# Kernel tuning notes

Measured on AMD Instinct MI355X. Metric: run time of the kernel, lower is better.

## Reference

```python
import jax, jax.numpy as jnp
import numpy as np

B, S, D, H = 4, 2048, 1024, 16
DK = D // H

def setup_inputs() -> dict:
    key = jax.random.key(0)
    ks = jax.random.split(key, 8)
    Q = jax.random.normal(ks[0], (B, S, D), dtype=jnp.float32)
    K = jax.random.normal(ks[1], (B, S, D), dtype=jnp.float32)
    V = jax.random.normal(ks[2], (B, S, D), dtype=jnp.float32)
    # causal mask: 0 means masked (as in masked_fill(mask == 0, -inf))
    mask = jnp.broadcast_to(jnp.tril(jnp.ones((S, S), dtype=jnp.int32))[None, None], (B, 1, S, S))
    scale = 1.0 / np.sqrt(D)
    W_Q = jax.random.normal(ks[3], (D, D), dtype=jnp.float32) * scale
    W_K = jax.random.normal(ks[4], (D, D), dtype=jnp.float32) * scale
    W_V = jax.random.normal(ks[5], (D, D), dtype=jnp.float32) * scale
    W_O = jax.random.normal(ks[6], (D, D), dtype=jnp.float32) * scale
    return {"Q": Q, "K": K, "V": V, "mask": mask,
            "W_Q": W_Q, "W_K": W_K, "W_V": W_V, "W_O": W_O}

def _split_heads(x):
    # [B, S, D] -> [B, H, S, DK]
    b, s, _ = x.shape
    return x.reshape(b, s, H, DK).transpose(0, 2, 1, 3)

def reference(Q, K, V, mask, W_Q, W_K, W_V, W_O):
    # nn.Linear(d,d,bias=False): y = x @ W.T ; here W_* stored as [D, D]
    q = _split_heads(Q @ W_Q.T)
    k = _split_heads(K @ W_K.T)
    v = _split_heads(V @ W_V.T)
    scores = jnp.einsum('bhqd,bhkd->bhqk', q, k) / jnp.sqrt(jnp.float32(DK))
    scores = jnp.where(mask == 0, -jnp.inf, scores)
    weights = jax.nn.softmax(scores, axis=-1)
    weights = jnp.nan_to_num(weights, nan=0.0)  # fully-masked rows -> 0
    # dropout is identity at eval / p=0
    attn = jnp.einsum('bhqk,bhkd->bhqd', weights, v)
    attn = attn.transpose(0, 2, 1, 3).reshape(Q.shape[0], Q.shape[1], D)
    return attn @ W_O.T
```

## Files before the change

### kernel.cpp

```cpp
#include <hip/hip_runtime.h>
#include <stdint.h>

#define B_  4
#define S_  2048
#define D_  1024
#define H_  16
#define DK_ 64

typedef __attribute__((ext_vector_type(8)))  short   short8;
typedef __attribute__((ext_vector_type(8)))  unsigned short ushort8;
typedef __attribute__((ext_vector_type(4)))  float   f32x4;
typedef __attribute__((ext_vector_type(16))) float   f32x16;

#define GPTR(p) ((const __attribute__((address_space(1))) void*)(p))
#define SPTR(p) ((__attribute__((address_space(3))) void*)(p))

__device__ inline unsigned short f2bf(float f) {
  uint32_t u = __float_as_uint(f);
  uint32_t r = (u + 0x7fffu + ((u >> 16) & 1u)) >> 16;
  return (unsigned short)r;
}
__device__ inline float bf2f(unsigned short h) {
  return __uint_as_float(((uint32_t)h) << 16);
}
__device__ inline uint32_t pkbf(float a, float b) {
  uint32_t r;
  asm("v_cvt_pk_bf16_f32 %0, %1, %2" : "=v"(r) : "v"(a), "v"(b));
  return r;
}
__device__ inline void pl32(uint32_t& a, uint32_t& b) {
  asm volatile("v_permlane32_swap_b32 %0, %1" : "+v"(a), "+v"(b));
}
__device__ inline short8 mk8(uint32_t a, uint32_t b, uint32_t c, uint32_t d) {
  union { uint32_t u[4]; short8 s; } x;
  x.u[0] = a; x.u[1] = b; x.u[2] = c; x.u[3] = d;
  return x.s;
}

__global__ __launch_bounds__(256) void conv_one(const float* __restrict__ src,
                                                unsigned short* __restrict__ dst,
                                                size_t n) {
  size_t i = ((size_t)blockIdx.x * blockDim.x + threadIdx.x) * 4;
  if (i < n) {
    float4 v = *reinterpret_cast<const float4*>(src + i);
    ushort4 o;
    o.x = f2bf(v.x); o.y = f2bf(v.y); o.z = f2bf(v.z); o.w = f2bf(v.w);
    *reinterpret_cast<ushort4*>(dst + i) = o;
  }
}

__global__ __launch_bounds__(256) void conv_x3(const float* __restrict__ q,
                                               const float* __restrict__ k,
                                               const float* __restrict__ v,
                                               unsigned short* __restrict__ dst) {
  const size_t NX = (size_t)B_ * S_ * D_;
  const float* src = (blockIdx.z == 0) ? q : (blockIdx.z == 1) ? k : v;
  unsigned short* d = dst + (size_t)blockIdx.z * NX;
  size_t i = ((size_t)blockIdx.x * blockDim.x + threadIdx.x) * 4;
  float4 vv = *reinterpret_cast<const float4*>(src + i);
  ushort4 o;
  o.x = f2bf(vv.x); o.y = f2bf(vv.y); o.z = f2bf(vv.z); o.w = f2bf(vv.w);
  *reinterpret_cast<ushort4*>(d + i) = o;
}

__global__ __launch_bounds__(256) void conv_w4(const float* __restrict__ w0,
                                               const float* __restrict__ w1,
                                               const float* __restrict__ w2,
                                               const float* __restrict__ w3,
                                               unsigned short* __restrict__ dst) {
  const size_t NW = (size_t)D_ * D_;
  const float* src = (blockIdx.z == 0) ? w0 : (blockIdx.z == 1) ? w1
                   : (blockIdx.z == 2) ? w2 : w3;
  unsigned short* d = dst + (size_t)blockIdx.z * NW;
  size_t i = ((size_t)blockIdx.x * blockDim.x + threadIdx.x) * 4;
  if (i < NW) {
    float4 v = *reinterpret_cast<const float4*>(src + i);
    ushort4 o;
    o.x = f2bf(v.x); o.y = f2bf(v.y); o.z = f2bf(v.z); o.w = f2bf(v.w);
    *reinterpret_cast<ushort4*>(d + i) = o;
  }
}

#define BM 128
#define BN 128
#define BK 32

__global__ __launch_bounds__(256) void gemm_qkv(const unsigned short* __restrict__ X0,
                                                const unsigned short* __restrict__ X1,
                                                const unsigned short* __restrict__ X2,
                                                const unsigned short* __restrict__ W,
                                                unsigned short* __restrict__ P,
                                                int zbase) {
  const size_t NW = (size_t)D_ * D_;
  const size_t NX = (size_t)B_ * S_ * D_;
  const int z = zbase + blockIdx.z;

  const unsigned short* A;
  const unsigned short* Bm;
  unsigned short* C;
  int N, m0, n0;
  if (z == 2) {
    A = W + 2 * NW; Bm = X2; C = P + 2 * NX;
    N = B_ * S_;
    m0 = (blockIdx.x & 7) * BM;
    n0 = (blockIdx.x >> 3) * BN;
  } else {
    A = z ? X1 : X0; Bm = W + (size_t)z * NW; C = P + (size_t)z * NX;
    N = D_;
    m0 = (blockIdx.x >> 3) * BM;
    n0 = (blockIdx.x & 7) * BN;
  }
  const int K = D_;

  __shared__ unsigned short sA[2][BM * BK];
  __shared__ unsigned short sB[2][BN * BK];

  const int tid  = threadIdx.x;
  const int lane = tid & 63;
  const int wid  = tid >> 6;
  const int wr   = wid >> 1, wc = wid & 1;
  const int g = lane >> 4, c = lane & 15;

  f32x4 acc[4][4];
#pragma unroll
  for (int m = 0; m < 4; ++m)
#pragma unroll
    for (int n = 0; n < 4; ++n) acc[m][n] = (f32x4){0.f, 0.f, 0.f, 0.f};

  auto stage = [&](int kt_, int bs) {
    const int k0 = kt_ * BK;
#pragma unroll
    for (int i = 0; i < 2; ++i) {
      const int ob  = i * 4096 + wid * 1024 + lane * 16;
      const int row = ob >> 6;
      const int cb  = ob & 63;
      const unsigned short* ga = A  + (size_t)(m0 + row) * K + k0 + (cb >> 1);
      const unsigned short* gb = Bm + (size_t)(n0 + row) * K + k0 + (cb >> 1);
      __builtin_amdgcn_global_load_lds(GPTR(ga), SPTR(&sA[bs][(i * 4096 + wid * 1024) >> 1]), 16, 0, 0);
      __builtin_amdgcn_global_load_lds(GPTR(gb), SPTR(&sB[bs][(i * 4096 + wid * 1024) >> 1]), 16, 0, 0);
    }
  };

  const int nkt = K / BK;
  stage(0, 0);
  __syncthreads();
  int cur = 0;
  for (int kt = 0; kt < nkt; ++kt) {
    if (kt + 1 < nkt) stage(kt + 1, cur ^ 1);

    short8 af[4], bf[4];
#pragma unroll
    for (int m = 0; m < 4; ++m)
      af[m] = *reinterpret_cast<const short8*>(&sA[cur][(wr * 64 + m * 16 + c) * BK + 8 * g]);
#pragma unroll
    for (int n = 0; n < 4; ++n)
      bf[n] = *reinterpret_cast<const short8*>(&sB[cur][(wc * 64 + n * 16 + c) * BK + 8 * g]);
#pragma unroll
    for (int m = 0; m < 4; ++m)
#pragma unroll
      for (int n = 0; n < 4; ++n)
        acc[m][n] = __builtin_amdgcn_mfma_f32_16x16x32_bf16(af[m], bf[n], acc[m][n], 0, 0, 0);
    __syncthreads();
    cur ^= 1;
  }

#pragma unroll
  for (int m = 0; m < 4; ++m)
#pragma unroll
    for (int n = 0; n < 4; ++n)
#pragma unroll
      for (int r = 0; r < 4; ++r) {
        const int row = m0 + wr * 64 + m * 16 + 4 * g + r;
        const int col = n0 + wc * 64 + n * 16 + c;
        C[(size_t)row * N + col] = f2bf(acc[m][n][r]);
      }
}

__global__ __launch_bounds__(256) void gemm_out(const unsigned short* __restrict__ A,
                                                const unsigned short* __restrict__ Bm,
                                                float* __restrict__ C,
                                                int M, int N, int K) {
  __shared__ unsigned short sA[2][BM * BK];
  __shared__ unsigned short sB[2][BN * BK];

  const int tid  = threadIdx.x;
  const int lane = tid & 63;
  const int wid  = tid >> 6;
  const int wr   = wid >> 1, wc = wid & 1;
  const int g = lane >> 4, c = lane & 15;

  const int m0 = blockIdx.y * BM;
  const int n0 = blockIdx.x * BN;

  f32x4 acc[4][4];
#pragma unroll
  for (int m = 0; m < 4; ++m)
#pragma unroll
    for (int n = 0; n < 4; ++n) acc[m][n] = (f32x4){0.f, 0.f, 0.f, 0.f};

  auto stage = [&](int kt_, int bs) {
    const int k0 = kt_ * BK;
#pragma unroll
    for (int i = 0; i < 2; ++i) {
      const int ob  = i * 4096 + wid * 1024 + lane * 16;
      const int row = ob >> 6;
      const int cb  = ob & 63;
      const unsigned short* ga = A  + (size_t)(m0 + row) * K + k0 + (cb >> 1);
      const unsigned short* gb = Bm + (size_t)(n0 + row) * K + k0 + (cb >> 1);
      __builtin_amdgcn_global_load_lds(GPTR(ga), SPTR(&sA[bs][(i * 4096 + wid * 1024) >> 1]), 16, 0, 0);
      __builtin_amdgcn_global_load_lds(GPTR(gb), SPTR(&sB[bs][(i * 4096 + wid * 1024) >> 1]), 16, 0, 0);
    }
  };

  const int nkt = K / BK;
  stage(0, 0);
  __syncthreads();
  int cur = 0;
  for (int kt = 0; kt < nkt; ++kt) {
    if (kt + 1 < nkt) stage(kt + 1, cur ^ 1);

    short8 af[4], bf[4];
#pragma unroll
    for (int m = 0; m < 4; ++m)
      af[m] = *reinterpret_cast<const short8*>(&sA[cur][(wr * 64 + m * 16 + c) * BK + 8 * g]);
#pragma unroll
    for (int n = 0; n < 4; ++n)
      bf[n] = *reinterpret_cast<const short8*>(&sB[cur][(wc * 64 + n * 16 + c) * BK + 8 * g]);
#pragma unroll
    for (int m = 0; m < 4; ++m)
#pragma unroll
      for (int n = 0; n < 4; ++n)
        acc[m][n] = __builtin_amdgcn_mfma_f32_16x16x32_bf16(af[m], bf[n], acc[m][n], 0, 0, 0);
    __syncthreads();
    cur ^= 1;
  }

#pragma unroll
  for (int m = 0; m < 4; ++m)
#pragma unroll
    for (int n = 0; n < 4; ++n)
#pragma unroll
      for (int r = 0; r < 4; ++r) {
        const int row = m0 + wr * 64 + m * 16 + 4 * g + r;
        const int col = n0 + wc * 64 + n * 16 + c;
        C[(size_t)row * N + col] = acc[m][n][r];
      }
}

__global__ __launch_bounds__(256, 4) void attn_fwd(const unsigned short* __restrict__ qp,
                                                   const unsigned short* __restrict__ kp,
                                                   const unsigned short* __restrict__ vtp,
                                                   unsigned short* __restrict__ attn) {
  const int bh = blockIdx.x;
  const int bx = blockIdx.y;
  const int b = bh >> 4, h = bh & 15;

  __shared__ unsigned short smem[4 * 64 * 64];

  const int tid  = threadIdx.x;
  const int lane = tid & 63;
  const int wid  = tid >> 6;
  const int hi   = lane >> 5;
  const int lo5  = lane & 31;

  const size_t headoff  = (size_t)b * S_ * D_ + (size_t)h * DK_;
  const size_t vheadoff = (size_t)(h * DK_) * (size_t)(B_ * S_) + (size_t)b * S_;

  const int xk = (lo5 & 7) << 4;

  auto stage = [&](int kt_, int bs) {
#pragma unroll
    for (int i = 0; i < 2; ++i) {
      const int base_ob = i * 4096 + wid * 1024;
      const int ob  = base_ob + lane * 16;
      const int row = ob >> 7;
      const int scb = (ob & 127) ^ ((row & 7) << 4);
      const unsigned short* gk = &kp[headoff + (size_t)(kt_ * 64 + row) * D_ + (scb >> 1)];
      const unsigned short* gv = &vtp[vheadoff + (size_t)row * (B_ * S_) + kt_ * 64 + (scb >> 1)];
      __builtin_amdgcn_global_load_lds(GPTR(gk), SPTR(&smem[bs * 4096 + (base_ob >> 1)]), 16, 0, 0);
      __builtin_amdgcn_global_load_lds(GPTR(gv), SPTR(&smem[8192 + bs * 4096 + (base_ob >> 1)]), 16, 0, 0);
    }
  };

#pragma unroll 1
  for (int pass = 0; pass < 2; ++pass) {
    const int qtile = pass ? bx : (15 - bx);
    const int qw = qtile * 128 + wid * 32;
    const int qg = qw + lo5;

    __syncthreads();

    short8 aq[4];
#pragma unroll
    for (int t = 0; t < 4; ++t) {
      ushort8 raw = *reinterpret_cast<const ushort8*>(
          &qp[headoff + (size_t)qg * D_ + t * 16 + hi * 8]);
      short8 sv;
#pragma unroll
      for (int j = 0; j < 8; ++j) sv[j] = (short)f2bf(bf2f(raw[j]) * 0.125f);
      aq[t] = sv;
    }

    float mrun = -3.0e38f, lrun = 0.f;
    f32x16 oa0, oa1;
#pragma unroll
    for (int r = 0; r < 16; ++r) { oa0[r] = 0.f; oa1[r] = 0.f; }

    const int nkv = 2 * (qtile + 1);
    stage(0, 0);

    for (int kt = 0; kt < nkv; ++kt) {
      const int cur = kt & 1;
      if (kt < nkv - 1) {
        stage(kt + 1, cur ^ 1);
        asm volatile("s_waitcnt vmcnt(4)" ::: "memory");
      } else {
        asm volatile("s_waitcnt vmcnt(0)" ::: "memory");
      }
      __builtin_amdgcn_sched_barrier(0);
      __builtin_amdgcn_s_barrier();
      __builtin_amdgcn_sched_barrier(0);

      const int kv0 = kt * 64;
      if (kv0 <= qw + 31) {
        const unsigned short* Kb = &smem[cur * 4096];
        const unsigned short* Vb = &smem[8192 + cur * 4096];

        f32x16 st0, st1;
#pragma unroll
        for (int r = 0; r < 16; ++r) { st0[r] = 0.f; st1[r] = 0.f; }
        __builtin_amdgcn_s_setprio(1);
#pragma unroll
        for (int t = 0; t < 4; ++t) {
          const int off = ((32 * t + 16 * hi) ^ xk) >> 1;
          short8 k0 = *reinterpret_cast<const short8*>(&Kb[lo5 * 64 + off]);
          short8 k1 = *reinterpret_cast<const short8*>(&Kb[(32 + lo5) * 64 + off]);
          st0 = __builtin_amdgcn_mfma_f32_32x32x16_bf16(k0, aq[t], st0, 0, 0, 0);
          st1 = __builtin_amdgcn_mfma_f32_32x32x16_bf16(k1, aq[t], st1, 0, 0, 0);
        }
        __builtin_amdgcn_s_setprio(0);

        if (kv0 + 63 > qw) {
#pragma unroll
          for (int r = 0; r < 16; ++r) {
            const int kvl = kv0 + (r & 3) + 8 * (r >> 2) + 4 * hi;
            if (kvl > qg)      st0[r] = -3.0e38f;
            if (kvl + 32 > qg) st1[r] = -3.0e38f;
          }
        }

        float tm = fmaxf(st0[0], st1[0]);
#pragma unroll
        for (int r = 1; r < 16; ++r) tm = fmaxf(tm, fmaxf(st0[r], st1[r]));
        tm = fmaxf(tm, __shfl_xor(tm, 32));
        const bool grow = !__all(tm <= mrun + 8.0f);
        float alpha = 1.0f;
        if (grow) {
          const float newm = fmaxf(mrun, tm);
          alpha = __expf(mrun - newm);
          mrun = newm;
        }

        float ls = 0.f;
#pragma unroll
        for (int r = 0; r < 16; ++r) { st0[r] = __expf(st0[r] - mrun); ls += st0[r]; }
        uint32_t a0 = pkbf(st0[0],  st0[1]),  a1 = pkbf(st0[2],  st0[3]);
        uint32_t b0 = pkbf(st0[4],  st0[5]),  b1 = pkbf(st0[6],  st0[7]);
        uint32_t c0 = pkbf(st0[8],  st0[9]),  c1 = pkbf(st0[10], st0[11]);
        uint32_t d0 = pkbf(st0[12], st0[13]), d1 = pkbf(st0[14], st0[15]);
        pl32(a0, b0); pl32(a1, b1);
        pl32(c0, d0); pl32(c1, d1);
        short8 pf0 = mk8(a0, a1, b0, b1);
        short8 pf1 = mk8(c0, c1, d0, d1);

#pragma unroll
        for (int r = 0; r < 16; ++r) { st1[r] = __expf(st1[r] - mrun); ls += st1[r]; }
        uint32_t e0 = pkbf(st1[0],  st1[1]),  e1 = pkbf(st1[2],  st1[3]);
        uint32_t f0 = pkbf(st1[4],  st1[5]),  f1 = pkbf(st1[6],  st1[7]);
        uint32_t g0 = pkbf(st1[8],  st1[9]),  g1 = pkbf(st1[10], st1[11]);
        uint32_t h0 = pkbf(st1[12], st1[13]), h1 = pkbf(st1[14], st1[15]);
        pl32(e0, f0); pl32(e1, f1);
        pl32(g0, h0); pl32(g1, h1);
        short8 pf2 = mk8(e0, e1, f0, f1);
        short8 pf3 = mk8(g0, g1, h0, h1);

        ls += __shfl_xor(ls, 32);
        if (grow) {
          lrun = lrun * alpha + ls;
#pragma unroll
          for (int r = 0; r < 16; ++r) { oa0[r] *= alpha; oa1[r] *= alpha; }
        } else {
          lrun += ls;
        }

        __builtin_amdgcn_s_setprio(1);
#pragma unroll
        for (int c4 = 0; c4 < 4; ++c4) {
          const int off = ((32 * c4 + 16 * hi) ^ xk) >> 1;
          short8 v0 = *reinterpret_cast<const short8*>(&Vb[lo5 * 64 + off]);
          short8 v1 = *reinterpret_cast<const short8*>(&Vb[(32 + lo5) * 64 + off]);
          const short8 pf = (c4 == 0) ? pf0 : (c4 == 1) ? pf1 : (c4 == 2) ? pf2 : pf3;
          oa0 = __builtin_amdgcn_mfma_f32_32x32x16_bf16(v0, pf, oa0, 0, 0, 0);
          oa1 = __builtin_amdgcn_mfma_f32_32x32x16_bf16(v1, pf, oa1, 0, 0, 0);
        }
        __builtin_amdgcn_s_setprio(0);
      }

      asm volatile("s_waitcnt lgkmcnt(0)" ::: "memory");
      __builtin_amdgcn_sched_barrier(0);
      __builtin_amdgcn_s_barrier();
      __builtin_amdgcn_sched_barrier(0);
    }

    {
      unsigned short* sO = &smem[wid * (32 * 72)];
      const float inv = 1.0f / lrun;
#pragma unroll
      for (int r = 0; r < 16; ++r) {
        const int dl = (r & 3) + 8 * (r >> 2) + 4 * hi;
        sO[lo5 * 72 + dl]      = f2bf(oa0[r] * inv);
        sO[lo5 * 72 + 32 + dl] = f2bf(oa1[r] * inv);
      }
      asm volatile("s_waitcnt lgkmcnt(0)" ::: "memory");
      const int row = lane >> 1, h2 = lane & 1;
      const unsigned short* src = &smem[wid * (32 * 72) + row * 72 + h2 * 32];
      unsigned short* dst = &attn[headoff + (size_t)(qtile * 128 + wid * 32 + row) * D_ + h2 * 32];
#pragma unroll
      for (int j = 0; j < 4; ++j)
        *reinterpret_cast<short8*>(dst + 8 * j) = *reinterpret_cast<const short8*>(src + 8 * j);
    }
  }
}

extern "C" void kernel_launch(void* const* d_in, const int* in_sizes, int n_in,
                              void* d_out, int out_size, void* d_ws, size_t ws_size,
                              hipStream_t stream) {
  const float* Q  = (const float*)d_in[0];
  const float* K  = (const float*)d_in[1];
  const float* V  = (const float*)d_in[2];
  const float* Wq = (const float*)d_in[4];
  const float* Wk = (const float*)d_in[5];
  const float* Wv = (const float*)d_in[6];
  const float* Wo = (const float*)d_in[7];
  float* out = (float*)d_out;

  const size_t NX = (size_t)B_ * S_ * D_;
  const size_t NW = (size_t)D_ * D_;

  const bool fused = ws_size >= 2 * (6 * NX + 4 * NW);

  unsigned short* ws = (unsigned short*)d_ws;
  unsigned short* Xq = ws;
  unsigned short* Xk = fused ? Xq + NX : Xq;
  unsigned short* Xv = fused ? Xk + NX : Xq;
  unsigned short* Wb = Xv + NX;
  unsigned short* Pj = Wb + 4 * NW;
  unsigned short* At = Xq;

  const int M = B_ * S_;
  dim3 blk(256);
  dim3 gridConvX((unsigned)(NX / 4 / 256), 1, 3);
  dim3 gridConvW((unsigned)(NW / 4 / 256), 1, 4);
  dim3 gridQKV(512, 1, 3);
  dim3 gridOut(D_ / BN, M / BM);
  dim3 gridAttn(B_ * H_, 8);

  conv_w4<<<gridConvW, blk, 0, stream>>>(Wq, Wk, Wv, Wo, Wb);

  if (fused) {
    conv_x3<<<gridConvX, blk, 0, stream>>>(Q, K, V, Xq);
    gemm_qkv<<<gridQKV, blk, 0, stream>>>(Xq, Xk, Xv, Wb, Pj, 0);
  } else {
    dim3 g1((unsigned)(NX / 4 / 256));
    dim3 gz(512, 1, 1);
    conv_one<<<g1, blk, 0, stream>>>(Q, Xq, NX);
    gemm_qkv<<<gz, blk, 0, stream>>>(Xq, Xq, Xq, Wb, Pj, 0);
    conv_one<<<g1, blk, 0, stream>>>(K, Xq, NX);
    gemm_qkv<<<gz, blk, 0, stream>>>(Xq, Xq, Xq, Wb, Pj, 1);
    conv_one<<<g1, blk, 0, stream>>>(V, Xq, NX);
    gemm_qkv<<<gz, blk, 0, stream>>>(Xq, Xq, Xq, Wb, Pj, 2);
  }

  attn_fwd<<<gridAttn, blk, 0, stream>>>(Pj, Pj + NX, Pj + 2 * NX, At);
  gemm_out<<<gridOut, blk, 0, stream>>>(At, Wb + 3 * NW, out, M, D_, D_);
}
```

Baseline: 208.9 us.

## Triple-buffer GEMM loads with explicit vmcnt waits, LDS swizzle, and block remap

Both bf16 GEMM kernels (QKV projection and output projection) move from a double-buffered to a triple-buffered global-to-LDS pipeline, prefetching two K-tiles ahead. Manual s_waitcnt vmcnt counts and raw s_barrier calls replace __syncthreads. An XOR swizzle on the LDS column chunk is meant to cut bank conflicts on the short8 fragment reads. MFMA sections run at raised wave priority, and the block index mapping is changed so consecutive blocks walk the M dimension, which alters L2 reuse of the weight tiles. The extra buffer raises LDS use per block, and the hand-counted vmcnt values must match the number of outstanding loads exactly.

```diff
diff --git a/kernel.cpp b/kernel.cpp
--- a/kernel.cpp
+++ b/kernel.cpp
@@ -102,18 +102,18 @@
   if (z == 2) {
     A = W + 2 * NW; Bm = X2; C = P + 2 * NX;
     N = B_ * S_;
-    m0 = (blockIdx.x & 7) * BM;
-    n0 = (blockIdx.x >> 3) * BN;
+    m0 = (blockIdx.x >> 6) * BM;
+    n0 = (blockIdx.x & 63) * BN;
   } else {
     A = z ? X1 : X0; Bm = W + (size_t)z * NW; C = P + (size_t)z * NX;
     N = D_;
-    m0 = (blockIdx.x >> 3) * BM;
-    n0 = (blockIdx.x & 7) * BN;
+    m0 = (blockIdx.x & 63) * BM;
+    n0 = (blockIdx.x >> 6) * BN;
   }
   const int K = D_;
 
-  __shared__ unsigned short sA[2][BM * BK];
-  __shared__ unsigned short sB[2][BN * BK];
+  __shared__ unsigned short sA[3][BM * BK];
+  __shared__ unsigned short sB[3][BN * BK];
 
   const int tid  = threadIdx.x;
   const int lane = tid & 63;
@@ -131,37 +131,59 @@
     const int k0 = kt_ * BK;
 #pragma unroll
     for (int i = 0; i < 2; ++i) {
-      const int ob  = i * 4096 + wid * 1024 + lane * 16;
+      const int base_ob = i * 4096 + wid * 1024;
+      const int ob  = base_ob + lane * 16;
       const int row = ob >> 6;
-      const int cb  = ob & 63;
-      const unsigned short* ga = A  + (size_t)(m0 + row) * K + k0 + (cb >> 1);
-      const unsigned short* gb = Bm + (size_t)(n0 + row) * K + k0 + (cb >> 1);
-      __builtin_amdgcn_global_load_lds(GPTR(ga), SPTR(&sA[bs][(i * 4096 + wid * 1024) >> 1]), 16, 0, 0);
-      __builtin_amdgcn_global_load_lds(GPTR(gb), SPTR(&sB[bs][(i * 4096 + wid * 1024) >> 1]), 16, 0, 0);
+      const int scb = (ob & 63) ^ (((ob >> 7) & 3) << 4);
+      const unsigned short* ga = A  + (size_t)(m0 + row) * K + k0 + (scb >> 1);
+      const unsigned short* gb = Bm + (size_t)(n0 + row) * K + k0 + (scb >> 1);
+      __builtin_amdgcn_global_load_lds(GPTR(ga), SPTR(&sA[bs][base_ob >> 1]), 16, 0, 0);
+      __builtin_amdgcn_global_load_lds(GPTR(gb), SPTR(&sB[bs][base_ob >> 1]), 16, 0, 0);
     }
   };
 
   const int nkt = K / BK;
   stage(0, 0);
-  __syncthreads();
-  int cur = 0;
+  stage(1, 1);
   for (int kt = 0; kt < nkt; ++kt) {
-    if (kt + 1 < nkt) stage(kt + 1, cur ^ 1);
+    const int cur = kt % 3;
+    if (kt + 2 < nkt) {
+      stage(kt + 2, (kt + 2) % 3);
+      asm volatile("s_waitcnt vmcnt(8)" ::: "memory");
+    } else if (kt + 1 < nkt) {
+      asm volatile("s_waitcnt vmcnt(4)" ::: "memory");
+    } else {
+      asm volatile("s_waitcnt vmcnt(0)" ::: "memory");
+    }
+    __builtin_amdgcn_sched_barrier(0);
+    __builtin_amdgcn_s_barrier();
+    __builtin_amdgcn_sched_barrier(0);
 
     short8 af[4], bf[4];
 #pragma unroll
-    for (int m = 0; m < 4; ++m)
-      af[m] = *reinterpret_cast<const short8*>(&sA[cur][(wr * 64 + m * 16 + c) * BK + 8 * g]);
-#pragma unroll
-    for (int n = 0; n < 4; ++n)
-      bf[n] = *reinterpret_cast<const short8*>(&sB[cur][(wc * 64 + n * 16 + c) * BK + 8 * g]);
+    for (int m = 0; m < 4; ++m) {
+      const int ra = wr * 64 + m * 16 + c;
+      af[m] = *reinterpret_cast<const short8*>(
+          &sA[cur][ra * BK + ((g ^ ((ra >> 1) & 3)) << 3)]);
+    }
+#pragma unroll
+    for (int n = 0; n < 4; ++n) {
+      const int rb = wc * 64 + n * 16 + c;
+      bf[n] = *reinterpret_cast<const short8*>(
+          &sB[cur][rb * BK + ((g ^ ((rb >> 1) & 3)) << 3)]);
+    }
+    __builtin_amdgcn_s_setprio(1);
 #pragma unroll
     for (int m = 0; m < 4; ++m)
 #pragma unroll
       for (int n = 0; n < 4; ++n)
         acc[m][n] = __builtin_amdgcn_mfma_f32_16x16x32_bf16(af[m], bf[n], acc[m][n], 0, 0, 0);
-    __syncthreads();
-    cur ^= 1;
+    __builtin_amdgcn_s_setprio(0);
+
+    asm volatile("s_waitcnt lgkmcnt(0)" ::: "memory");
+    __builtin_amdgcn_sched_barrier(0);
+    __builtin_amdgcn_s_barrier();
+    __builtin_amdgcn_sched_barrier(0);
   }
 
 #pragma unroll
@@ -180,8 +202,8 @@
                                                 const unsigned short* __restrict__ Bm,
                                                 float* __restrict__ C,
                                                 int M, int N, int K) {
-  __shared__ unsigned short sA[2][BM * BK];
-  __shared__ unsigned short sB[2][BN * BK];
+  __shared__ unsigned short sA[3][BM * BK];
+  __shared__ unsigned short sB[3][BN * BK];
 
   const int tid  = threadIdx.x;
   const int lane = tid & 63;
@@ -189,8 +211,8 @@
   const int wr   = wid >> 1, wc = wid & 1;
   const int g = lane >> 4, c = lane & 15;
 
-  const int m0 = blockIdx.y * BM;
-  const int n0 = blockIdx.x * BN;
+  const int m0 = blockIdx.x * BM;
+  const int n0 = blockIdx.y * BN;
 
   f32x4 acc[4][4];
 #pragma unroll
@@ -202,37 +224,59 @@
     const int k0 = kt_ * BK;
 #pragma unroll
     for (int i = 0; i < 2; ++i) {
-      const int ob  = i * 4096 + wid * 1024 + lane * 16;
+      const int base_ob = i * 4096 + wid * 1024;
+      const int ob  = base_ob + lane * 16;
       const int row = ob >> 6;
-      const int cb  = ob & 63;
-      const unsigned short* ga = A  + (size_t)(m0 + row) * K + k0 + (cb >> 1);
-      const unsigned short* gb = Bm + (size_t)(n0 + row) * K + k0 + (cb >> 1);
-      __builtin_amdgcn_global_load_lds(GPTR(ga), SPTR(&sA[bs][(i * 4096 + wid * 1024) >> 1]), 16, 0, 0);
-      __builtin_amdgcn_global_load_lds(GPTR(gb), SPTR(&sB[bs][(i * 4096 + wid * 1024) >> 1]), 16, 0, 0);
+      const int scb = (ob & 63) ^ (((ob >> 7) & 3) << 4);
+      const unsigned short* ga = A  + (size_t)(m0 + row) * K + k0 + (scb >> 1);
+      const unsigned short* gb = Bm + (size_t)(n0 + row) * K + k0 + (scb >> 1);
+      __builtin_amdgcn_global_load_lds(GPTR(ga), SPTR(&sA[bs][base_ob >> 1]), 16, 0, 0);
+      __builtin_amdgcn_global_load_lds(GPTR(gb), SPTR(&sB[bs][base_ob >> 1]), 16, 0, 0);
     }
   };
 
   const int nkt = K / BK;
   stage(0, 0);
-  __syncthreads();
-  int cur = 0;
+  stage(1, 1);
   for (int kt = 0; kt < nkt; ++kt) {
-    if (kt + 1 < nkt) stage(kt + 1, cur ^ 1);
+    const int cur = kt % 3;
+    if (kt + 2 < nkt) {
+      stage(kt + 2, (kt + 2) % 3);
+      asm volatile("s_waitcnt vmcnt(8)" ::: "memory");
+    } else if (kt + 1 < nkt) {
+      asm volatile("s_waitcnt vmcnt(4)" ::: "memory");
+    } else {
+      asm volatile("s_waitcnt vmcnt(0)" ::: "memory");
+    }
+    __builtin_amdgcn_sched_barrier(0);
+    __builtin_amdgcn_s_barrier();
+    __builtin_amdgcn_sched_barrier(0);
 
     short8 af[4], bf[4];
 #pragma unroll
-    for (int m = 0; m < 4; ++m)
-      af[m] = *reinterpret_cast<const short8*>(&sA[cur][(wr * 64 + m * 16 + c) * BK + 8 * g]);
-#pragma unroll
-    for (int n = 0; n < 4; ++n)
-      bf[n] = *reinterpret_cast<const short8*>(&sB[cur][(wc * 64 + n * 16 + c) * BK + 8 * g]);
+    for (int m = 0; m < 4; ++m) {
+      const int ra = wr * 64 + m * 16 + c;
+      af[m] = *reinterpret_cast<const short8*>(
+          &sA[cur][ra * BK + ((g ^ ((ra >> 1) & 3)) << 3)]);
+    }
+#pragma unroll
+    for (int n = 0; n < 4; ++n) {
+      const int rb = wc * 64 + n * 16 + c;
+      bf[n] = *reinterpret_cast<const short8*>(
+          &sB[cur][rb * BK + ((g ^ ((rb >> 1) & 3)) << 3)]);
+    }
+    __builtin_amdgcn_s_setprio(1);
 #pragma unroll
     for (int m = 0; m < 4; ++m)
 #pragma unroll
       for (int n = 0; n < 4; ++n)
         acc[m][n] = __builtin_amdgcn_mfma_f32_16x16x32_bf16(af[m], bf[n], acc[m][n], 0, 0, 0);
-    __syncthreads();
-    cur ^= 1;
+    __builtin_amdgcn_s_setprio(0);
+
+    asm volatile("s_waitcnt lgkmcnt(0)" ::: "memory");
+    __builtin_amdgcn_sched_barrier(0);
+    __builtin_amdgcn_s_barrier();
+    __builtin_amdgcn_sched_barrier(0);
   }
 
 #pragma unroll
@@ -462,7 +506,7 @@
   dim3 gridConvX((unsigned)(NX / 4 / 256), 1, 3);
   dim3 gridConvW((unsigned)(NW / 4 / 256), 1, 4);
   dim3 gridQKV(512, 1, 3);
-  dim3 gridOut(D_ / BN, M / BM);
+  dim3 gridOut(M / BM, D_ / BN);
   dim3 gridAttn(B_ * H_, 8);
 
   conv_w4<<<gridConvW, blk, 0, stream>>>(Wq, Wk, Wv, Wo, Wb);
```

New measurement: 190.9 us. -8.6%, faster.
